# Optimization experiments

Measured on AMD Instinct MI355X. Metric: run time of the kernel, lower is better.

The kernel has to match this reference:

```python
import jax, jax.numpy as jnp
import numpy as np

N = 1_000_000
D = 256
S = 10_000  # num segments (graphs)


def setup_inputs() -> dict:
    key = jax.random.key(0)
    k1, k2 = jax.random.split(key)
    feats = jax.random.normal(k1, (N, D), dtype=jnp.float32)
    segment_ids = jnp.sort(jax.random.randint(k2, (N,), 0, S, dtype=jnp.int64))
    return {"feats": feats, "segment_ids": segment_ids, "num_segments": S}


def reference(feats, segment_ids, num_segments):
    # Segment-mean pooling: equivalent to the per-batch gather + mean + cat loop,
    # where node_batches partitions rows of feats and segment_ids encodes batch membership.
    sums = jax.ops.segment_sum(feats, segment_ids, num_segments=num_segments,
                               indices_are_sorted=True)  # [S, D]
    counts = jax.ops.segment_sum(jnp.ones((feats.shape[0],), dtype=feats.dtype),
                                 segment_ids, num_segments=num_segments,
                                 indices_are_sorted=True)  # [S]
    return sums / jnp.maximum(counts, 1.0)[:, None]
```

## Files before the change

### kernel.cpp

```cpp
#include <hip/hip_runtime.h>


#define DCOLS 256
#define D4    64

__global__ void seg_starts_kernel(const int* __restrict__ ids, int N, int S,
                                  int* __restrict__ starts) {
    int s = blockIdx.x * blockDim.x + threadIdx.x;
    if (s > S) return;
    int lo = 0, hi = N;
    while (lo < hi) {
        int mid = (lo + hi) >> 1;
        if (ids[mid] < s) lo = mid + 1;
        else hi = mid;
    }
    starts[s] = lo;
}

__global__ __launch_bounds__(256) void seg_mean_kernel(
        const float* __restrict__ feats,
        const int* __restrict__ starts,
        float* __restrict__ out) {
    const int s     = blockIdx.x;
    const int start = starts[s];
    const int end   = starts[s + 1];
    const int count = end - start;

    const int cg = threadIdx.x & 63;
    const int rg = threadIdx.x >> 6;

    const float4* f4 = reinterpret_cast<const float4*>(feats);

    float4 acc = make_float4(0.f, 0.f, 0.f, 0.f);
    for (int r = start + rg; r < end; r += 4) {
        float4 v = f4[(size_t)r * D4 + cg];
        acc.x += v.x; acc.y += v.y; acc.z += v.z; acc.w += v.w;
    }

    __shared__ float4 buf[256];
    buf[threadIdx.x] = acc;
    __syncthreads();

    if (threadIdx.x < 64) {
        float4 a = buf[threadIdx.x];
        float4 b = buf[threadIdx.x + 64];
        float4 c = buf[threadIdx.x + 128];
        float4 d = buf[threadIdx.x + 192];
        float cnt = (float)(count > 0 ? count : 1);
        float4 o;
        o.x = (a.x + b.x + c.x + d.x) / cnt;
        o.y = (a.y + b.y + c.y + d.y) / cnt;
        o.z = (a.z + b.z + c.z + d.z) / cnt;
        o.w = (a.w + b.w + c.w + d.w) / cnt;
        reinterpret_cast<float4*>(out)[(size_t)s * D4 + threadIdx.x] = o;
    }
}

extern "C" void kernel_launch(void* const* d_in, const int* in_sizes, int n_in,
                              void* d_out, int out_size, void* d_ws, size_t ws_size,
                              hipStream_t stream) {
    const float* feats = (const float*)d_in[0];
    const int*   ids   = (const int*)d_in[1];
    const int S = out_size / DCOLS;
    const int N = in_sizes[0] / DCOLS;

    int* starts = (int*)d_ws;

    int t = S + 1;
    seg_starts_kernel<<<(t + 255) / 256, 256, 0, stream>>>(ids, N, S, starts);

    seg_mean_kernel<<<S, 256, 0, stream>>>(feats, starts, (float*)d_out);
}
```

Baseline: 195.5 us.

## Fuse segment-boundary search into a one-wave-per-segment mean kernel

Removes the separate binary-search kernel and its workspace round trip. Each wave now finds its own segment start and end with a per-lane search and shares them by shuffle. Each segment gets one wave instead of a four-wave block, which drops the shared-memory reduction and the barrier. The row loop is unrolled four times with independent accumulators to keep more loads in flight. The cost is a redundant binary search per wave and fewer rows loaded in parallel per segment.

```diff
diff --git a/kernel.cpp b/kernel.cpp
--- a/kernel.cpp
+++ b/kernel.cpp
@@ -4,56 +4,57 @@
 #define DCOLS 256
 #define D4    64
 
-__global__ void seg_starts_kernel(const int* __restrict__ ids, int N, int S,
-                                  int* __restrict__ starts) {
-    int s = blockIdx.x * blockDim.x + threadIdx.x;
-    if (s > S) return;
+__global__ __launch_bounds__(256) void seg_mean_wave(
+        const float* __restrict__ feats,
+        const int* __restrict__ ids,
+        int N, int S,
+        float* __restrict__ out) {
+    const int wave = threadIdx.x >> 6;
+    const int lane = threadIdx.x & 63;
+    const int s    = blockIdx.x * 4 + wave;
+    if (s >= S) return;
+
+    const int target = s + (lane & 1);
     int lo = 0, hi = N;
     while (lo < hi) {
         int mid = (lo + hi) >> 1;
-        if (ids[mid] < s) lo = mid + 1;
+        if (ids[mid] < target) lo = mid + 1;
         else hi = mid;
     }
-    starts[s] = lo;
-}
-
-__global__ __launch_bounds__(256) void seg_mean_kernel(
-        const float* __restrict__ feats,
-        const int* __restrict__ starts,
-        float* __restrict__ out) {
-    const int s     = blockIdx.x;
-    const int start = starts[s];
-    const int end   = starts[s + 1];
+    const int start = __shfl(lo, 0, 64);
+    const int end   = __shfl(lo, 1, 64);
     const int count = end - start;
-
-    const int cg = threadIdx.x & 63;
-    const int rg = threadIdx.x >> 6;
 
     const float4* f4 = reinterpret_cast<const float4*>(feats);
 
-    float4 acc = make_float4(0.f, 0.f, 0.f, 0.f);
-    for (int r = start + rg; r < end; r += 4) {
-        float4 v = f4[(size_t)r * D4 + cg];
-        acc.x += v.x; acc.y += v.y; acc.z += v.z; acc.w += v.w;
+    float4 a0 = make_float4(0.f, 0.f, 0.f, 0.f);
+    float4 a1 = make_float4(0.f, 0.f, 0.f, 0.f);
+    float4 a2 = make_float4(0.f, 0.f, 0.f, 0.f);
+    float4 a3 = make_float4(0.f, 0.f, 0.f, 0.f);
+
+    int r = start;
+    for (; r + 3 < end; r += 4) {
+        float4 v0 = f4[(size_t)(r + 0) * D4 + lane];
+        float4 v1 = f4[(size_t)(r + 1) * D4 + lane];
+        float4 v2 = f4[(size_t)(r + 2) * D4 + lane];
+        float4 v3 = f4[(size_t)(r + 3) * D4 + lane];
+        a0.x += v0.x; a0.y += v0.y; a0.z += v0.z; a0.w += v0.w;
+        a1.x += v1.x; a1.y += v1.y; a1.z += v1.z; a1.w += v1.w;
+        a2.x += v2.x; a2.y += v2.y; a2.z += v2.z; a2.w += v2.w;
+        a3.x += v3.x; a3.y += v3.y; a3.z += v3.z; a3.w += v3.w;
+    }
+    for (; r < end; ++r) {
+        float4 v = f4[(size_t)r * D4 + lane];
+        a0.x += v.x; a0.y += v.y; a0.z += v.z; a0.w += v.w;
     }
 
-    __shared__ float4 buf[256];
-    buf[threadIdx.x] = acc;
-    __syncthreads();
-
-    if (threadIdx.x < 64) {
-        float4 a = buf[threadIdx.x];
-        float4 b = buf[threadIdx.x + 64];
-        float4 c = buf[threadIdx.x + 128];
-        float4 d = buf[threadIdx.x + 192];
-        float cnt = (float)(count > 0 ? count : 1);
-        float4 o;
-        o.x = (a.x + b.x + c.x + d.x) / cnt;
-        o.y = (a.y + b.y + c.y + d.y) / cnt;
-        o.z = (a.z + b.z + c.z + d.z) / cnt;
-        o.w = (a.w + b.w + c.w + d.w) / cnt;
-        reinterpret_cast<float4*>(out)[(size_t)s * D4 + threadIdx.x] = o;
-    }
+    const float cnt = (float)(count > 0 ? count : 1);
+    float4 o;
+    o.x = (a0.x + a1.x + a2.x + a3.x) / cnt;
+    o.y = (a0.y + a1.y + a2.y + a3.y) / cnt;
+    o.z = (a0.z + a1.z + a2.z + a3.z) / cnt;
+    o.w = (a0.w + a1.w + a2.w + a3.w) / cnt;
+    reinterpret_cast<float4*>(out)[(size_t)s * D4 + lane] = o;
 }
 
 extern "C" void kernel_launch(void* const* d_in, const int* in_sizes, int n_in,
@@ -64,10 +65,6 @@
     const int S = out_size / DCOLS;
     const int N = in_sizes[0] / DCOLS;
 
-    int* starts = (int*)d_ws;
-
-    int t = S + 1;
-    seg_starts_kernel<<<(t + 255) / 256, 256, 0, stream>>>(ids, N, S, starts);
-
-    seg_mean_kernel<<<S, 256, 0, stream>>>(feats, starts, (float*)d_out);
+    const int blocks = (S + 3) / 4;
+    seg_mean_wave<<<blocks, 256, 0, stream>>>(feats, ids, N, S, (float*)d_out);
 }
```

Result: slower. 200.1 us (+2.3%).
